# Optimization experiments

Hardware: AMD Instinct MI355X
Metric: run time of the kernel (lower is better)

The kernel has to match this reference:

```python
import jax, jax.numpy as jnp
import numpy as np

EMBED_DIM = 1024
N_HEAD = 16

def setup_inputs() -> dict:
    key = jax.random.key(0)
    ks = jax.random.split(key, 5)
    C = EMBED_DIM
    x = jax.random.normal(ks[0], (2, 2048, C), dtype=jnp.float32)
    s = 1.0 / np.sqrt(C)
    W_attn = jax.random.normal(ks[1], (C, 3 * C), dtype=jnp.float32) * s
    b_attn = jnp.zeros((3 * C,), dtype=jnp.float32)
    W_proj = jax.random.normal(ks[2], (C, C), dtype=jnp.float32) * s
    b_proj = jnp.zeros((C,), dtype=jnp.float32)
    return {"x": x, "W_attn": W_attn, "b_attn": b_attn, "W_proj": W_proj, "b_proj": b_proj}

def reference(x, W_attn, b_attn, W_proj, b_proj):
    B, T, C = x.shape
    H = N_HEAD
    D = C // H
    qkv = x @ W_attn + b_attn                      # [B,T,3C]
    q, k, v = jnp.split(qkv, 3, axis=-1)
    # [B,H,T,D]
    q = q.reshape(B, T, H, D).transpose(0, 2, 1, 3)
    k = k.reshape(B, T, H, D).transpose(0, 2, 1, 3)
    v = v.reshape(B, T, H, D).transpose(0, 2, 1, 3)
    att = jnp.einsum('bhqd,bhkd->bhqk', q, k) * (1.0 / jnp.sqrt(jnp.asarray(D, x.dtype)))
    causal = jnp.tril(jnp.ones((T, T), dtype=bool))
    att = jnp.where(causal, att, -jnp.inf)
    att = jax.nn.softmax(att, axis=-1)
    y = jnp.einsum('bhqk,bhkd->bhqd', att, v)      # [B,H,T,D]
    y = y.transpose(0, 2, 1, 3).reshape(B, T, C)
    return y @ W_proj + b_proj
```

## Files before the change

### kernel.cpp

```cpp
#include <hip/hip_runtime.h>
#include <stdint.h>

typedef __attribute__((ext_vector_type(4))) float f32x4;
typedef __attribute__((ext_vector_type(8))) __bf16 bf16x8;
typedef __attribute__((ext_vector_type(8))) unsigned short u16x8;

__device__ __forceinline__ unsigned short f2b(float f) {
  unsigned u = __float_as_uint(f);
  u += 0x7FFFu + ((u >> 16) & 1u);
  return (unsigned short)(u >> 16);
}
__device__ __forceinline__ float b2f(unsigned short s) {
  unsigned u = (unsigned)s << 16;
  return __uint_as_float(u);
}
__device__ __forceinline__ unsigned cvtpk_bf16(float lo, float hi) {
  unsigned r;
  asm("v_cvt_pk_bf16_f32 %0, %1, %2" : "=v"(r) : "v"(lo), "v"(hi));
  return r;
}

__device__ __forceinline__ void gload_lds16(const void* g, void* l) {
  typedef __attribute__((address_space(1))) void GV1;
  typedef __attribute__((address_space(3))) void LV3;
  __builtin_amdgcn_global_load_lds((GV1*)(void*)g, (LV3*)l, 16, 0, 0);
}

__device__ __forceinline__ void tile_barrier_keep4() {
  asm volatile("s_waitcnt vmcnt(4)" ::: "memory");
  __builtin_amdgcn_sched_barrier(0);
  __builtin_amdgcn_s_barrier();
  __builtin_amdgcn_sched_barrier(0);
}
__device__ __forceinline__ void tile_barrier_keep2() {
  asm volatile("s_waitcnt vmcnt(2)" ::: "memory");
  __builtin_amdgcn_sched_barrier(0);
  __builtin_amdgcn_s_barrier();
  __builtin_amdgcn_sched_barrier(0);
}
__device__ __forceinline__ void tile_barrier_keep0() {
  asm volatile("s_waitcnt vmcnt(0)" ::: "memory");
  __builtin_amdgcn_sched_barrier(0);
  __builtin_amdgcn_s_barrier();
  __builtin_amdgcn_sched_barrier(0);
}

__global__ __launch_bounds__(256) void convert_f32_bf16(const float* __restrict__ in,
                                                        unsigned short* __restrict__ out, int n) {
  int i = (blockIdx.x * 256 + threadIdx.x) * 8;
  if (i >= n) return;
  float4 a = *(const float4*)(in + i);
  float4 b = *(const float4*)(in + i + 4);
  u16x8 r;
  r[0] = f2b(a.x); r[1] = f2b(a.y); r[2] = f2b(a.z); r[3] = f2b(a.w);
  r[4] = f2b(b.x); r[5] = f2b(b.y); r[6] = f2b(b.z); r[7] = f2b(b.w);
  *(u16x8*)(out + i) = r;
}

__global__ __launch_bounds__(256) void transpose_f32_bf16(const float* __restrict__ W,
                                                          unsigned short* __restrict__ Wt,
                                                          int K, int N) {
  __shared__ unsigned short tile[32][33];
  int n0 = blockIdx.x * 32, k0 = blockIdx.y * 32;
  int tx = threadIdx.x, ty = threadIdx.y;
  #pragma unroll
  for (int j = 0; j < 32; j += 8)
    tile[ty + j][tx] = f2b(W[(size_t)(k0 + ty + j) * N + n0 + tx]);
  __syncthreads();
  #pragma unroll
  for (int j = 0; j < 32; j += 8)
    Wt[(size_t)(n0 + ty + j) * K + k0 + tx] = tile[tx][ty + j];
}

template <bool OUT_BF16, bool VSPLIT>
__global__ __launch_bounds__(256) void gemm_bt(const unsigned short* __restrict__ A,
                                               const unsigned short* __restrict__ Bt,
                                               const float* __restrict__ bias,
                                               void* __restrict__ Cout,
                                               unsigned short* __restrict__ vT,
                                               int M, int N, int K) {
  __shared__ unsigned short SMEM[24576];
  const int m0 = blockIdx.x * 128, n0 = blockIdx.y * 128;
  const int tid = threadIdx.x;
  const int w = tid >> 6, l = tid & 63;
  const int wm = w >> 1, wn = w & 1;
  const int c = l & 15, g = l >> 4;
  const int NT = K >> 5;
  const unsigned short* aptr[2];
  const unsigned short* bptr[2];
  #pragma unroll
  for (int i = 0; i < 2; ++i) {
    int rb = w * 32 + i * 16;
    aptr[i] = A  + (size_t)(m0 + rb + (l >> 2)) * K + (l & 3) * 8;
    bptr[i] = Bt + (size_t)(n0 + rb + (l >> 2)) * K + (l & 3) * 8;
  }
  f32x4 acc[4][4] = {};
  #pragma unroll
  for (int i = 0; i < 2; ++i) {
    int rb = w * 32 + i * 16;
    gload_lds16(aptr[i], &SMEM[rb * 32]);
    gload_lds16(bptr[i], &SMEM[4096 + rb * 32]);
  }
  if (NT > 1) {
    #pragma unroll
    for (int i = 0; i < 2; ++i) {
      int rb = w * 32 + i * 16;
      gload_lds16(aptr[i] + 32, &SMEM[8192 + rb * 32]);
      gload_lds16(bptr[i] + 32, &SMEM[8192 + 4096 + rb * 32]);
    }
    tile_barrier_keep4();
  } else {
    tile_barrier_keep0();
  }
  int cur = 0;
  for (int t = 0; t < NT; ++t) {
    const bool pre2 = (t + 2 < NT);
    if (pre2) {
      int sb = cur + 2; if (sb >= 3) sb -= 3;
      #pragma unroll
      for (int i = 0; i < 2; ++i) {
        int rb = w * 32 + i * 16;
        gload_lds16(aptr[i] + (size_t)(t + 2) * 32, &SMEM[sb * 8192 + rb * 32]);
        gload_lds16(bptr[i] + (size_t)(t + 2) * 32, &SMEM[sb * 8192 + 4096 + rb * 32]);
      }
    }
    const unsigned short* Ab = &SMEM[cur * 8192];
    const unsigned short* Bb = &SMEM[cur * 8192 + 4096];
    bf16x8 af[4], bf[4];
    #pragma unroll
    for (int mi = 0; mi < 4; ++mi)
      af[mi] = *(const bf16x8*)&Ab[(wm * 64 + mi * 16 + c) * 32 + g * 8];
    #pragma unroll
    for (int ni = 0; ni < 4; ++ni)
      bf[ni] = *(const bf16x8*)&Bb[(wn * 64 + ni * 16 + c) * 32 + g * 8];
    __builtin_amdgcn_s_setprio(1);
    #pragma unroll
    for (int mi = 0; mi < 4; ++mi)
      #pragma unroll
      for (int ni = 0; ni < 4; ++ni)
        acc[mi][ni] = __builtin_amdgcn_mfma_f32_16x16x32_bf16(af[mi], bf[ni], acc[mi][ni], 0, 0, 0);
    __builtin_amdgcn_s_setprio(0);
    if (t + 1 < NT) {
      if (pre2) tile_barrier_keep4();
      else      tile_barrier_keep0();
    }
    cur = (cur + 1 == 3) ? 0 : cur + 1;
  }
  if (VSPLIT && n0 >= 2048) {
    __syncthreads();
    unsigned short* TR = SMEM;
    #pragma unroll
    for (int mi = 0; mi < 4; ++mi)
      #pragma unroll
      for (int ni = 0; ni < 4; ++ni) {
        int cl = wn * 64 + ni * 16 + c;
        float bv = bias[n0 + cl];
        int rlb = wm * 64 + mi * 16 + 4 * g;
        ushort4 o4;
        o4.x = f2b(acc[mi][ni][0] + bv); o4.y = f2b(acc[mi][ni][1] + bv);
        o4.z = f2b(acc[mi][ni][2] + bv); o4.w = f2b(acc[mi][ni][3] + bv);
        *(ushort4*)&TR[cl * 136 + rlb] = o4;
      }
    __syncthreads();
    const int d0 = n0 - 2048;
    #pragma unroll
    for (int p = 0; p < 8; ++p) {
      int rowl = p * 16 + (tid >> 4);
      *(u16x8*)(vT + (size_t)(d0 + rowl) * 4096 + m0 + (tid & 15) * 8) =
          *(const u16x8*)&TR[rowl * 136 + (tid & 15) * 8];
    }
    return;
  }
  const int NS = VSPLIT ? 2048 : N;
  #pragma unroll
  for (int mi = 0; mi < 4; ++mi) {
    #pragma unroll
    for (int ni = 0; ni < 4; ++ni) {
      int colg = n0 + wn * 64 + ni * 16 + c;
      float bv = bias[colg];
      #pragma unroll
      for (int r = 0; r < 4; ++r) {
        int rowg = m0 + wm * 64 + mi * 16 + 4 * g + r;
        float v = acc[mi][ni][r] + bv;
        if (OUT_BF16)
          ((unsigned short*)Cout)[(size_t)rowg * NS + colg] = f2b(v);
        else
          ((float*)Cout)[(size_t)rowg * NS + colg] = v;
      }
    }
  }
}

__global__ __launch_bounds__(512) void attn_kernel(const unsigned short* __restrict__ qk,
                                                   const unsigned short* __restrict__ vT,
                                                   unsigned short* __restrict__ partO,
                                                   float* __restrict__ partML) {
  __shared__ unsigned short K_lds[3][64 * 64];
  __shared__ unsigned short V_lds[3][64 * 64];
  const int bid = blockIdx.x;
  const int bh = bid & 31;
  const int cid = 39 - (bid >> 5);
  int qt, ct;
  if (cid < 4)       { qt = cid;            ct = 0; }
  else if (cid < 12) { int e = cid - 4;  qt = 4 + (e >> 1);  ct = e & 1; }
  else if (cid < 24) { int e = cid - 12; int q3 = e / 3; qt = 8 + q3; ct = e - 3 * q3; }
  else               { int e = cid - 24; qt = 12 + (e >> 2); ct = e & 3; }
  const int ntt = 2 * qt + 2;
  const int t0 = ct * 8;
  const int ntl = min(ntt - t0, 8);
  const int b = bh >> 4, h = bh & 15;
  const int tid = threadIdx.x, w = tid >> 6, l = tid & 63;
  const int c = l & 15, g = l >> 4;
  const int hi = g >> 1;
  const int srcA = c + ((g & 1) << 5);
  const int srcB = srcA + 16;
  const size_t row0 = (size_t)b * 2048;
  const float SCL = 0.18033688f;
  const int KSTRIDE = 64 * 2048;
  const int VSTRIDE = 64;

  const int q0w = qt * 128 + w * 16;
  const int qg = q0w + c;

  bf16x8 qf[2];
  #pragma unroll
  for (int ks = 0; ks < 2; ++ks)
    qf[ks] = *(const bf16x8*)(qk + (row0 + qg) * 2048 + h * 64 + ks * 32 + g * 8);

  f32x4 acc[4] = {};
  float mstate = -1e30f, lstate = 0.f;

  const int krow = w * 8 + (l >> 3);
  const int kch = (l & 7) ^ (krow & 7);
  const unsigned short* kptr = qk + (row0 + t0 * 64 + krow) * 2048 + 1024 + h * 64 + kch * 8;
  const unsigned short* vptr = vT + (size_t)(h * 64 + krow) * 4096 + (b * 2048 + t0 * 64) + kch * 8;
  const int kdst = (w * 8) * 64;

  gload_lds16(kptr, &K_lds[0][kdst]);
  gload_lds16(vptr, &V_lds[0][kdst]);
  if (ntl > 1) {
    gload_lds16(kptr + KSTRIDE, &K_lds[1][kdst]);
    gload_lds16(vptr + VSTRIDE, &V_lds[1][kdst]);
    tile_barrier_keep2();
  } else {
    tile_barrier_keep0();
  }

  int cur = 0;
  for (int lt = 0; lt < ntl; ++lt) {
    const int kv0 = (t0 + lt) * 64;
    const bool pre2 = (lt + 2 < ntl);
    if (pre2) {
      int sb = cur + 2; if (sb >= 3) sb -= 3;
      gload_lds16(kptr + 2 * KSTRIDE, &K_lds[sb][kdst]);
      gload_lds16(vptr + 2 * VSTRIDE, &V_lds[sb][kdst]);
    }
    kptr += KSTRIDE;
    vptr += VSTRIDE;
    if (kv0 <= q0w + 15) {
      const char* Kb = (const char*)K_lds[cur];
      const char* Vb = (const char*)V_lds[cur];
      f32x4 s[4] = {};
      #pragma unroll
      for (int ks = 0; ks < 2; ++ks) {
        bf16x8 kf[4];
        #pragma unroll
        for (int nk = 0; nk < 4; ++nk) {
          int row = nk * 16 + c;
          kf[nk] = *(const bf16x8*)(Kb + row * 128 + ((ks * 64 + g * 16) ^ ((row & 7) << 4)));
        }
        __builtin_amdgcn_s_setprio(1);
        #pragma unroll
        for (int nk = 0; nk < 4; ++nk)
          s[nk] = __builtin_amdgcn_mfma_f32_16x16x32_bf16(kf[nk], qf[ks], s[nk], 0, 0, 0);
        __builtin_amdgcn_s_setprio(0);
      }
      if (kv0 + 63 > q0w) {
        #pragma unroll
        for (int nk = 0; nk < 4; ++nk)
          #pragma unroll
          for (int r = 0; r < 4; ++r) {
            int kvg = kv0 + nk * 16 + 4 * g + r;
            if (kvg > qg) s[nk][r] = -1e30f;
          }
      }
      float a0 = fmaxf(fmaxf(s[0][0], s[0][1]), fmaxf(s[0][2], s[0][3]));
      float a1 = fmaxf(fmaxf(s[1][0], s[1][1]), fmaxf(s[1][2], s[1][3]));
      float a2 = fmaxf(fmaxf(s[2][0], s[2][1]), fmaxf(s[2][2], s[2][3]));
      float a3 = fmaxf(fmaxf(s[3][0], s[3][1]), fmaxf(s[3][2], s[3][3]));
      float mx = fmaxf(fmaxf(a0, a1), fmaxf(a2, a3));
      mx = fmaxf(mx, __shfl_xor(mx, 16));
      mx = fmaxf(mx, __shfl_xor(mx, 32));
      if (!__all(mx <= mstate)) {
        float mnew = fmaxf(mstate, mx);
        float alpha = exp2f((mstate - mnew) * SCL);
        mstate = mnew;
        lstate *= alpha;
        #pragma unroll
        for (int nd = 0; nd < 4; ++nd) acc[nd] *= alpha;
      }
      float ms = mstate * SCL;
      #pragma unroll
      for (int nk = 0; nk < 4; ++nk) {
        #pragma unroll
        for (int r = 0; r < 4; ++r) s[nk][r] = exp2f(fmaf(s[nk][r], SCL, -ms));
        lstate += (s[nk][0] + s[nk][1]) + (s[nk][2] + s[nk][3]);
      }
      unsigned pk[4][2];
      #pragma unroll
      for (int nk = 0; nk < 4; ++nk) {
        pk[nk][0] = cvtpk_bf16(s[nk][0], s[nk][1]);
        pk[nk][1] = cvtpk_bf16(s[nk][2], s[nk][3]);
      }
      #pragma unroll
      for (int vks = 0; vks < 2; ++vks) {
        unsigned rA00 = __shfl(pk[2 * vks][0], srcA, 64);
        unsigned rA01 = __shfl(pk[2 * vks][1], srcA, 64);
        unsigned rA10 = __shfl(pk[2 * vks + 1][0], srcA, 64);
        unsigned rA11 = __shfl(pk[2 * vks + 1][1], srcA, 64);
        unsigned rB00 = __shfl(pk[2 * vks][0], srcB, 64);
        unsigned rB01 = __shfl(pk[2 * vks][1], srcB, 64);
        unsigned rB10 = __shfl(pk[2 * vks + 1][0], srcB, 64);
        unsigned rB11 = __shfl(pk[2 * vks + 1][1], srcB, 64);
        union { unsigned u[4]; bf16x8 v; } pa;
        pa.u[0] = hi ? rA10 : rA00;
        pa.u[1] = hi ? rA11 : rA01;
        pa.u[2] = hi ? rB10 : rB00;
        pa.u[3] = hi ? rB11 : rB01;
        bf16x8 vf[4];
        #pragma unroll
        for (int nd = 0; nd < 4; ++nd) {
          int row = nd * 16 + c;
          vf[nd] = *(const bf16x8*)(Vb + row * 128 + ((vks * 64 + g * 16) ^ ((row & 7) << 4)));
        }
        __builtin_amdgcn_s_setprio(1);
        #pragma unroll
        for (int nd = 0; nd < 4; ++nd)
          acc[nd] = __builtin_amdgcn_mfma_f32_16x16x32_bf16(vf[nd], pa.v, acc[nd], 0, 0, 0);
        __builtin_amdgcn_s_setprio(0);
      }
    }
    if (lt + 1 < ntl) {
      if (pre2) tile_barrier_keep2();
      else      tile_barrier_keep0();
    }
    cur = (cur + 1 == 3) ? 0 : cur + 1;
  }

  float lsum = lstate;
  lsum += __shfl_xor(lsum, 16);
  lsum += __shfl_xor(lsum, 32);
  const int qrow = w * 16 + c;
  #pragma unroll
  for (int nd = 0; nd < 4; ++nd) {
    ushort4 o4;
    o4.x = f2b(acc[nd][0]); o4.y = f2b(acc[nd][1]);
    o4.z = f2b(acc[nd][2]); o4.w = f2b(acc[nd][3]);
    *(ushort4*)(partO + (size_t)bid * 8192 + qrow * 64 + nd * 16 + 4 * g) = o4;
  }
  if (g == 0) {
    partML[(size_t)bid * 256 + qrow * 2 + 0] = mstate;
    partML[(size_t)bid * 256 + qrow * 2 + 1] = lsum;
  }
}

__global__ __launch_bounds__(256) void attn_combine(const unsigned short* __restrict__ partO,
                                                    const float* __restrict__ partML,
                                                    unsigned short* __restrict__ out) {
  const int bid = blockIdx.x;
  const int qt = bid >> 5, bh = bid & 31;
  const int b = bh >> 4, h = bh & 15;
  const int np = (2 * qt + 9) >> 3;
  const int base = (qt < 4) ? qt
                 : (qt < 8) ? 4 + 2 * (qt - 4)
                 : (qt < 12) ? 12 + 3 * (qt - 8)
                 : 24 + 4 * (qt - 12);
  const int t = threadIdx.x;
  const int row = t >> 1, cg = (t & 1) * 32;
  const float SCL = 0.18033688f;
  float mstar = -1e30f;
  #pragma unroll
  for (int p = 0; p < 4; ++p)
    if (p < np)
      mstar = fmaxf(mstar, partML[(size_t)(((39 - (base + p)) << 5) | bh) * 256 + row * 2]);
  float L = 0.f;
  float o[32];
  #pragma unroll
  for (int j = 0; j < 32; ++j) o[j] = 0.f;
  #pragma unroll
  for (int p = 0; p < 4; ++p) {
    if (p < np) {
      int slot = ((39 - (base + p)) << 5) | bh;
      float mp = partML[(size_t)slot * 256 + row * 2 + 0];
      float lp = partML[(size_t)slot * 256 + row * 2 + 1];
      float wgt = exp2f((mp - mstar) * SCL);
      L = fmaf(wgt, lp, L);
      const unsigned short* src = partO + (size_t)slot * 8192 + row * 64 + cg;
      #pragma unroll
      for (int q = 0; q < 4; ++q) {
        u16x8 a = *(const u16x8*)(src + q * 8);
        #pragma unroll
        for (int j = 0; j < 8; ++j)
          o[q * 8 + j] = fmaf(b2f(a[j]), wgt, o[q * 8 + j]);
      }
    }
  }
  float rinv = 1.0f / L;
  size_t trow = (size_t)b * 2048 + qt * 128 + row;
  #pragma unroll
  for (int q = 0; q < 4; ++q) {
    u16x8 r;
    #pragma unroll
    for (int j = 0; j < 8; ++j) r[j] = f2b(o[q * 8 + j] * rinv);
    *(u16x8*)(out + trow * 1024 + h * 64 + cg + q * 8) = r;
  }
}

extern "C" void kernel_launch(void* const* d_in, const int* in_sizes, int n_in,
                              void* d_out, int out_size, void* d_ws, size_t ws_size,
                              hipStream_t stream) {
  const float* x      = (const float*)d_in[0];
  const float* W_attn = (const float*)d_in[1];
  const float* b_attn = (const float*)d_in[2];
  const float* W_proj = (const float*)d_in[3];
  const float* b_proj = (const float*)d_in[4];
  float* out = (float*)d_out;

  char* ws = (char*)d_ws;
  unsigned short* Wproj_t  = (unsigned short*)(ws + 0);
  unsigned short* qk       = (unsigned short*)(ws + 2097152);
  unsigned short* vT       = (unsigned short*)(ws + 18874368);
  unsigned short* x_bf     = (unsigned short*)(ws + 27262976);
  unsigned short* Wattn_t  = (unsigned short*)(ws + 35651584);
  unsigned short* partO    = (unsigned short*)(ws + 27262976);
  unsigned short* attn_out = (unsigned short*)(ws + 48234496);
  float*          partML   = (float*)(ws + 56623104);

  convert_f32_bf16<<<2048, 256, 0, stream>>>(x, x_bf, 4194304);
  transpose_f32_bf16<<<dim3(96, 32), dim3(32, 8), 0, stream>>>(W_attn, Wattn_t, 1024, 3072);
  transpose_f32_bf16<<<dim3(32, 32), dim3(32, 8), 0, stream>>>(W_proj, Wproj_t, 1024, 1024);

  gemm_bt<true, true><<<dim3(32, 24), 256, 0, stream>>>(x_bf, Wattn_t, b_attn, qk, vT,
                                                        4096, 3072, 1024);
  attn_kernel<<<1280, 512, 0, stream>>>(qk, vT, partO, partML);
  attn_combine<<<512, 256, 0, stream>>>(partO, partML, attn_out);
  gemm_bt<false, false><<<dim3(32, 8), 256, 0, stream>>>(attn_out, Wproj_t, b_proj, out, nullptr,
                                                         4096, 1024, 1024);
}
```

Baseline: 134.8 us.

## Use 256x256-tile QKV GEMM with swizzled LDS and separate V transpose

Replaces the 128x128 QKV projection GEMM with a 512-thread 256x256-tile kernel. The new kernel uses double-buffered LDS with an XOR swizzle and a block-index remap so neighbouring blocks share tiles in cache. The fused in-epilogue V transpose is removed: V is written row-major to a temporary buffer and then transposed by a separate bf16 transpose kernel. The larger tiles raise arithmetic intensity and cut redundant global loads, but the grid drops to 192 blocks, which may underfill the GPU's compute units. The extra transpose launch also adds a round trip through memory.

```diff
diff --git a/kernel.cpp b/kernel.cpp
--- a/kernel.cpp
+++ b/kernel.cpp
@@ -72,12 +72,118 @@
     Wt[(size_t)(n0 + ty + j) * K + k0 + tx] = tile[tx][ty + j];
 }
 
-template <bool OUT_BF16, bool VSPLIT>
+__global__ __launch_bounds__(256) void transpose_bf16(const unsigned short* __restrict__ in,
+                                                      unsigned short* __restrict__ out,
+                                                      int K, int N) {
+  __shared__ unsigned short tile[32][33];
+  int n0 = blockIdx.x * 32, k0 = blockIdx.y * 32;
+  int tx = threadIdx.x, ty = threadIdx.y;
+  #pragma unroll
+  for (int j = 0; j < 32; j += 8)
+    tile[ty + j][tx] = in[(size_t)(k0 + ty + j) * N + n0 + tx];
+  __syncthreads();
+  #pragma unroll
+  for (int j = 0; j < 32; j += 8)
+    out[(size_t)(n0 + ty + j) * K + k0 + tx] = tile[tx][ty + j];
+}
+
+__global__ __launch_bounds__(512) void gemm256(const unsigned short* __restrict__ A,
+                                               const unsigned short* __restrict__ Bt,
+                                               const float* __restrict__ bias,
+                                               unsigned short* __restrict__ qk,
+                                               unsigned short* __restrict__ vtmp) {
+  constexpr int K = 1024, NT = 16;
+  __shared__ unsigned short SMEM[65536];
+  const int id = blockIdx.x;
+  const int sw = (id & 7) * 24 + (id >> 3);
+  const int bx = sw & 15, by = sw >> 4;
+  const int m0 = bx * 256, n0 = by * 256;
+  const int tid = threadIdx.x;
+  const int w = tid >> 6, l = tid & 63;
+  const int wm = w >> 2, wn = w & 3;
+  const int c = l & 15, g = l >> 4;
+  const int sc = (c ^ (c >> 2)) & 3;
+  const int srow = tid >> 2;
+  const int sch = (tid & 3) ^ ((srow ^ (srow >> 2)) & 3);
+  const unsigned short* aS0 = A  + (size_t)(m0 + srow) * K + sch * 8;
+  const unsigned short* aS1 = A  + (size_t)(m0 + 128 + srow) * K + sch * 8;
+  const unsigned short* bS0 = Bt + (size_t)(n0 + srow) * K + sch * 8;
+  const unsigned short* bS1 = Bt + (size_t)(n0 + 128 + srow) * K + sch * 8;
+  const int wdst = w * 512;
+
+  f32x4 acc[8][4] = {};
+
+  #pragma unroll
+  for (int p = 0; p < 2; ++p) {
+    gload_lds16(aS0 + p * 32, &SMEM[p * 8192 + wdst]);
+    gload_lds16(aS1 + p * 32, &SMEM[p * 8192 + 4096 + wdst]);
+    gload_lds16(bS0 + p * 32, &SMEM[16384 + p * 8192 + wdst]);
+    gload_lds16(bS1 + p * 32, &SMEM[16384 + p * 8192 + 4096 + wdst]);
+  }
+
+  int curbuf = 0;
+  for (int j = 0; j < NT; ++j) {
+    const bool nlast = (j + 1 < NT);
+    const unsigned short* cb = &SMEM[curbuf * 32768];
+    unsigned short* nb = &SMEM[(curbuf ^ 1) * 32768];
+    #pragma unroll
+    for (int p = 0; p < 2; ++p) {
+      if (nlast || p == 0) tile_barrier_keep4();
+      else                 tile_barrier_keep0();
+      if (nlast) {
+        const int co = (j + 1) * 64 + p * 32;
+        gload_lds16(aS0 + co, &nb[p * 8192 + wdst]);
+        gload_lds16(aS1 + co, &nb[p * 8192 + 4096 + wdst]);
+        gload_lds16(bS0 + co, &nb[16384 + p * 8192 + wdst]);
+        gload_lds16(bS1 + co, &nb[16384 + p * 8192 + 4096 + wdst]);
+      }
+      const unsigned short* Ab = cb + p * 8192;
+      const unsigned short* Bb = cb + 16384 + p * 8192;
+      bf16x8 af[8], bf[4];
+      #pragma unroll
+      for (int mi = 0; mi < 8; ++mi) {
+        int row = wm * 128 + mi * 16 + c;
+        af[mi] = *(const bf16x8*)&Ab[row * 32 + ((g ^ sc) << 3)];
+      }
+      #pragma unroll
+      for (int ni = 0; ni < 4; ++ni) {
+        int row = wn * 64 + ni * 16 + c;
+        bf[ni] = *(const bf16x8*)&Bb[row * 32 + ((g ^ sc) << 3)];
+      }
+      __builtin_amdgcn_s_setprio(1);
+      #pragma unroll
+      for (int mi = 0; mi < 8; ++mi)
+        #pragma unroll
+        for (int ni = 0; ni < 4; ++ni)
+          acc[mi][ni] = __builtin_amdgcn_mfma_f32_16x16x32_bf16(af[mi], bf[ni], acc[mi][ni], 0, 0, 0);
+      __builtin_amdgcn_s_setprio(0);
+    }
+    curbuf ^= 1;
+  }
+
+  const bool isV = (n0 >= 2048);
+  #pragma unroll
+  for (int mi = 0; mi < 8; ++mi) {
+    #pragma unroll
+    for (int ni = 0; ni < 4; ++ni) {
+      int colg = n0 + wn * 64 + ni * 16 + c;
+      float bv = bias[colg];
+      #pragma unroll
+      for (int r = 0; r < 4; ++r) {
+        int rowg = m0 + wm * 128 + mi * 16 + 4 * g + r;
+        float v = acc[mi][ni][r] + bv;
+        if (isV) vtmp[(size_t)rowg * 1024 + colg - 2048] = f2b(v);
+        else     qk[(size_t)rowg * 2048 + colg] = f2b(v);
+      }
+    }
+  }
+}
+
+template <bool OUT_BF16>
 __global__ __launch_bounds__(256) void gemm_bt(const unsigned short* __restrict__ A,
                                                const unsigned short* __restrict__ Bt,
                                                const float* __restrict__ bias,
                                                void* __restrict__ Cout,
-                                               unsigned short* __restrict__ vT,
                                                int M, int N, int K) {
   __shared__ unsigned short SMEM[24576];
   const int m0 = blockIdx.x * 128, n0 = blockIdx.y * 128;
@@ -146,32 +252,6 @@
     }
     cur = (cur + 1 == 3) ? 0 : cur + 1;
   }
-  if (VSPLIT && n0 >= 2048) {
-    __syncthreads();
-    unsigned short* TR = SMEM;
-    #pragma unroll
-    for (int mi = 0; mi < 4; ++mi)
-      #pragma unroll
-      for (int ni = 0; ni < 4; ++ni) {
-        int cl = wn * 64 + ni * 16 + c;
-        float bv = bias[n0 + cl];
-        int rlb = wm * 64 + mi * 16 + 4 * g;
-        ushort4 o4;
-        o4.x = f2b(acc[mi][ni][0] + bv); o4.y = f2b(acc[mi][ni][1] + bv);
-        o4.z = f2b(acc[mi][ni][2] + bv); o4.w = f2b(acc[mi][ni][3] + bv);
-        *(ushort4*)&TR[cl * 136 + rlb] = o4;
-      }
-    __syncthreads();
-    const int d0 = n0 - 2048;
-    #pragma unroll
-    for (int p = 0; p < 8; ++p) {
-      int rowl = p * 16 + (tid >> 4);
-      *(u16x8*)(vT + (size_t)(d0 + rowl) * 4096 + m0 + (tid & 15) * 8) =
-          *(const u16x8*)&TR[rowl * 136 + (tid & 15) * 8];
-    }
-    return;
-  }
-  const int NS = VSPLIT ? 2048 : N;
   #pragma unroll
   for (int mi = 0; mi < 4; ++mi) {
     #pragma unroll
@@ -183,9 +263,9 @@
         int rowg = m0 + wm * 64 + mi * 16 + 4 * g + r;
         float v = acc[mi][ni][r] + bv;
         if (OUT_BF16)
-          ((unsigned short*)Cout)[(size_t)rowg * NS + colg] = f2b(v);
+          ((unsigned short*)Cout)[(size_t)rowg * N + colg] = f2b(v);
         else
-          ((float*)Cout)[(size_t)rowg * NS + colg] = v;
+          ((float*)Cout)[(size_t)rowg * N + colg] = v;
       }
     }
   }
@@ -434,16 +514,16 @@
   unsigned short* Wattn_t  = (unsigned short*)(ws + 35651584);
   unsigned short* partO    = (unsigned short*)(ws + 27262976);
   unsigned short* attn_out = (unsigned short*)(ws + 48234496);
+  unsigned short* vtmp     = (unsigned short*)(ws + 48234496);
   float*          partML   = (float*)(ws + 56623104);
 
   convert_f32_bf16<<<2048, 256, 0, stream>>>(x, x_bf, 4194304);
   transpose_f32_bf16<<<dim3(96, 32), dim3(32, 8), 0, stream>>>(W_attn, Wattn_t, 1024, 3072);
   transpose_f32_bf16<<<dim3(32, 32), dim3(32, 8), 0, stream>>>(W_proj, Wproj_t, 1024, 1024);
 
-  gemm_bt<true, true><<<dim3(32, 24), 256, 0, stream>>>(x_bf, Wattn_t, b_attn, qk, vT,
-                                                        4096, 3072, 1024);
+  gemm256<<<192, 512, 0, stream>>>(x_bf, Wattn_t, b_attn, qk, vtmp);
+  transpose_bf16<<<dim3(32, 128), dim3(32, 8), 0, stream>>>(vtmp, vT, 4096, 1024);
   attn_kernel<<<1280, 512, 0, stream>>>(qk, vT, partO, partML);
   attn_combine<<<512, 256, 0, stream>>>(partO, partML, attn_out);
-  gemm_bt<false, false><<<dim3(32, 8), 256, 0, stream>>>(attn_out, Wproj_t, b_proj, out, nullptr,
-                                                         4096, 1024, 1024);
-}
+  gemm_bt<false><<<dim3(32, 8), 256, 0, stream>>>(attn_out, Wproj_t, b_proj, out, 4096, 1024, 1024);
+}
```

After: 135.9 us. About the same (+0.8%).
